# Kernel optimization log

Measured on AMD Instinct MI355X. Metric: run time of the kernel, lower is better.

## Reference

```python
import jax, jax.numpy as jnp
import numpy as np

D_MODEL = 1024
N_HEADS = 16
D_K = D_MODEL // N_HEADS
THETA = 10000.0
SEQ = 2048
BATCH = 2


def setup_inputs() -> dict:
    key = jax.random.key(0)
    ks = jax.random.split(key, 5)
    std = (2.0 / (D_MODEL + D_MODEL)) ** 0.5
    return {
        "x": jax.random.normal(ks[0], (BATCH, SEQ, D_MODEL), dtype=jnp.float32),
        "token_positions": jnp.arange(SEQ, dtype=jnp.int64 if jax.config.jax_enable_x64 else jnp.int32),
        "wq": jax.random.normal(ks[1], (D_MODEL, D_MODEL), dtype=jnp.float32) * std,
        "wk": jax.random.normal(ks[2], (D_MODEL, D_MODEL), dtype=jnp.float32) * std,
        "wv": jax.random.normal(ks[3], (D_MODEL, D_MODEL), dtype=jnp.float32) * std,
        "wo": jax.random.normal(ks[4], (D_MODEL, D_MODEL), dtype=jnp.float32) * std,
    }


def _apply_rope(t, token_positions):
    # t: [b, h, s, d_k]; interleaved even/odd rotation (RoPE)
    k = jnp.arange(D_K // 2, dtype=t.dtype)
    inv_freq = THETA ** (-2.0 * k / D_K)                     # [d_k/2]
    angles = token_positions.astype(t.dtype)[:, None] * inv_freq  # [s, d_k/2]
    cos, sin = jnp.cos(angles), jnp.sin(angles)
    even, odd = t[..., 0::2], t[..., 1::2]
    re = even * cos - odd * sin
    ro = odd * cos + even * sin
    # re-interleave: stack last then reshape back to [..., d_k]
    return jnp.stack([re, ro], axis=-1).reshape(t.shape)


def reference(x, token_positions, wq, wk, wv, wo):
    b, s, _ = x.shape
    def proj(w):
        y = jnp.einsum("bsd,ed->bse", x, w)               # Linear: x @ W^T
        return y.reshape(b, s, N_HEADS, D_K).transpose(0, 2, 1, 3)  # [b,h,s,dk]
    q, k, v = proj(wq), proj(wk), proj(wv)
    q = _apply_rope(q, token_positions)
    k = _apply_rope(k, token_positions)
    scores = jnp.einsum("bhqd,bhkd->bhqk", q, k) / jnp.sqrt(jnp.asarray(D_K, x.dtype))
    attn = jax.nn.softmax(scores, axis=-1)
    out = jnp.einsum("bhqk,bhkd->bhqd", attn, v)          # [b,h,s,dk]
    out = out.transpose(0, 2, 1, 3).reshape(b, s, D_MODEL)
    return jnp.einsum("bsd,ed->bse", out, wo)
```

## Files before the change

kernel.cpp:

```cpp
#include <hip/hip_runtime.h>
#include <stdint.h>

typedef __bf16 bf16x8 __attribute__((ext_vector_type(8)));
typedef __bf16 bf16x2 __attribute__((ext_vector_type(2)));
typedef float f32x4 __attribute__((ext_vector_type(4)));
typedef float f32x16 __attribute__((ext_vector_type(16)));
typedef unsigned short ushort_t;
typedef unsigned int uint;

#define SEQ    2048
#define DMODEL 1024
#define NHEAD  16
#define DKH    64
#define NBATCH 2
#define MROWS  (NBATCH*SEQ)
#define LOG2E  1.44269504088896340736f

__device__ __forceinline__ uint pk2(float a, float b) {
  bf16x2 t; t[0] = (__bf16)a; t[1] = (__bf16)b;
  return __builtin_bit_cast(uint, t);
}
__device__ __forceinline__ ushort_t b1(float a) {
  return __builtin_bit_cast(ushort_t, (__bf16)a);
}
__device__ __forceinline__ float fexp2(float x) {
#if __has_builtin(__builtin_amdgcn_exp2f)
  return __builtin_amdgcn_exp2f(x);
#else
  return exp2f(x);
#endif
}

__device__ __forceinline__ void gload16(const void* g, void* l) {
  __builtin_amdgcn_global_load_lds(
      (const __attribute__((address_space(1))) void*)g,
      (__attribute__((address_space(3))) void*)l, 16, 0, 0);
}

__device__ __forceinline__ f32x4 mfma16(bf16x8 a, bf16x8 b, f32x4 c) {
  return __builtin_amdgcn_mfma_f32_16x16x32_bf16(a, b, c, 0, 0, 0);
}
__device__ __forceinline__ f32x16 mfma32(bf16x8 a, bf16x8 b, f32x16 c) {
  return __builtin_amdgcn_mfma_f32_32x32x16_bf16(a, b, c, 0, 0, 0);
}

__global__ __launch_bounds__(256) void cvt_all(
    const float* __restrict__ x, const float* __restrict__ wq,
    const float* __restrict__ wk, const float* __restrict__ wv,
    const float* __restrict__ wo, uint2* __restrict__ out)
{
  int b = blockIdx.x;
  const float4* src; uint2* dst; int i;
  if (b < 4096) {
    i = b * 256 + threadIdx.x; src = (const float4*)x; dst = out;
  } else {
    int s = (b - 4096) >> 10;
    i = ((b - 4096) & 1023) * 256 + threadIdx.x;
    src = (const float4*)(s == 0 ? wq : s == 1 ? wk : s == 2 ? wv : wo);
    dst = out + (size_t)1048576 + (size_t)s * 262144;
  }
  float4 v = src[i];
  uint2 r; r.x = pk2(v.x, v.y); r.y = pk2(v.z, v.w);
  dst[i] = r;
}

__global__ __launch_bounds__(256) void rope_tab_kernel(const int* __restrict__ tokpos, float2* __restrict__ tab) {
  int t = blockIdx.x * 256 + threadIdx.x;
  int s = t >> 5, k = t & 31;
  double inv = pow(10000.0, -(double)(2 * k) / 64.0);
  double ang = (double)tokpos[s] * inv;
  tab[t] = make_float2((float)cos(ang), (float)sin(ang));
}

__global__ __launch_bounds__(256) void gemm_nt(
    const ushort_t* __restrict__ A, const ushort_t* __restrict__ W,
    const float2* __restrict__ tab,
    ushort_t* __restrict__ Qo, ushort_t* __restrict__ Ko, ushort_t* __restrict__ Vo,
    float* __restrict__ outf, int fused)
{
  __shared__ ushort_t lA[2][128 * 64];
  __shared__ ushort_t lB[2][128 * 64];
  const int tid = threadIdx.x;
  const int w = tid >> 6, l = tid & 63, lo = l & 15, hi = l >> 4;
  const int wr = (w >> 1) * 64, wc = (w & 1) * 64;
  const char* Ab = (const char*)A + (size_t)blockIdx.y * 128 * 2048;
  const char* Bb = (const char*)W + (size_t)blockIdx.x * 128 * 2048;
  f32x4 acc[4][4] = {};

  const int o0 = w * 1024 + l * 16;
  const int r0 = o0 >> 7;
  const int us = ((o0 >> 4) & 7) ^ (r0 & 7);
  const char* ap = Ab + (size_t)r0 * 2048 + us * 16;
  const char* bp = Bb + (size_t)r0 * 2048 + us * 16;

  auto stage = [&](char* dA, char* dB, const char* aq, const char* bq) {
    #pragma unroll
    for (int i = 0; i < 4; ++i) {
      gload16(aq + i * 65536, dA + w * 1024 + i * 4096);
      gload16(bq + i * 65536, dB + w * 1024 + i * 4096);
    }
  };
  auto comp = [&](const ushort_t* lAb, const ushort_t* lBb) {
    #pragma unroll
    for (int c = 0; c < 2; ++c) {
      bf16x8 af[4], wf[4];
      #pragma unroll
      for (int m = 0; m < 4; ++m) {
        int row = wr + m * 16 + lo;
        af[m] = *(const bf16x8*)((const char*)lAb + row * 128 + ((c * 64 + hi * 16) ^ ((row & 7) << 4)));
      }
      #pragma unroll
      for (int n = 0; n < 4; ++n) {
        int row = wc + n * 16 + lo;
        wf[n] = *(const bf16x8*)((const char*)lBb + row * 128 + ((c * 64 + hi * 16) ^ ((row & 7) << 4)));
      }
      #pragma unroll
      for (int m = 0; m < 4; ++m)
        #pragma unroll
        for (int n = 0; n < 4; ++n)
          acc[m][n] = mfma16(af[m], wf[n], acc[m][n]);
    }
  };

  stage((char*)lA[0], (char*)lB[0], ap, bp); ap += 128; bp += 128;
  __syncthreads();
  for (int it = 0; it < 16; it += 2) {
    stage((char*)lA[1], (char*)lB[1], ap, bp); ap += 128; bp += 128;
    comp(lA[0], lB[0]);
    __syncthreads();
    if (it + 2 < 16) { stage((char*)lA[0], (char*)lB[0], ap, bp); ap += 128; bp += 128; }
    comp(lA[1], lB[1]);
    __syncthreads();
  }

  const int mode = fused ? (blockIdx.x >> 3) : 3;
  const int colblk = fused ? (blockIdx.x & 7) : blockIdx.x;
  const int rowbase = blockIdx.y * 128 + wr + hi * 4;
  const int colbase = colblk * 128 + wc + lo;

  if (mode == 3) {
    #pragma unroll
    for (int m = 0; m < 4; ++m)
      #pragma unroll
      for (int n = 0; n < 4; ++n) {
        int e = colbase + n * 16;
        #pragma unroll
        for (int r = 0; r < 4; ++r) {
          int row = rowbase + m * 16 + r;
          outf[(size_t)row * 1024 + e] = acc[m][n][r];
        }
      }
    return;
  }
  if (mode == 2) {
    #pragma unroll
    for (int m = 0; m < 4; ++m) {
      int row0 = rowbase + m * 16;
      int b = row0 >> 11, s = row0 & 2047;
      #pragma unroll
      for (int n = 0; n < 4; ++n) {
        int e = colbase + n * 16;
        int h = e >> 6, dk = e & 63;
        uint2 pk;
        pk.x = pk2(acc[m][n][0], acc[m][n][1]);
        pk.y = pk2(acc[m][n][2], acc[m][n][3]);
        *(uint2*)(Vo + ((size_t)((b * NHEAD + h) * DKH + dk) * SEQ + s)) = pk;
      }
    }
    return;
  }
  ushort_t* outb = (mode == 0) ? Qo : Ko;
  const float qscale = (mode == 0) ? (0.125f * LOG2E) : 1.0f;
  #pragma unroll
  for (int m = 0; m < 4; ++m) {
    #pragma unroll
    for (int n = 0; n < 4; ++n) {
      int e = colbase + n * 16;
      int h = e >> 6, dk = e & 63, kf = dk >> 1;
      float sgn = (e & 1) ? 1.0f : -1.0f;
      #pragma unroll
      for (int r = 0; r < 4; ++r) {
        int row = rowbase + m * 16 + r;
        int s = row & 2047, b = row >> 11;
        float2 cs = tab[s * 32 + kf];
        float v = acc[m][n][r];
        float p = __shfl_xor(v, 1, 64);
        float res = (v * cs.x + sgn * p * cs.y) * qscale;
        outb[((size_t)((b * NHEAD + h) * SEQ + s)) * DKH + dk] = b1(res);
      }
    }
  }
}

__global__ __launch_bounds__(128) void attn_fwd(
    const ushort_t* __restrict__ Qg, const ushort_t* __restrict__ Kg,
    const ushort_t* __restrict__ VTg, ushort_t* __restrict__ attn)
{
  __shared__ char lds[65536];
  const int tid = threadIdx.x;
  const int w = tid >> 6, l = tid & 63;
  const int q31 = l & 31, hf = l >> 5, s7 = l & 7;
  const int bh = blockIdx.y;
  const int q0 = blockIdx.x * 128 + w * 64;
  const char* Kb = (const char*)Kg + (size_t)bh * 2048 * 128;
  const char* Vb = (const char*)VTg + (size_t)bh * 64 * 4096;

  bf16x8 qreg[2][4];
  #pragma unroll
  for (int qb = 0; qb < 2; ++qb) {
    const ushort_t* qp = Qg + ((size_t)bh * 2048 + q0 + qb * 32 + q31) * 64 + hf * 8;
    #pragma unroll
    for (int c = 0; c < 4; ++c) qreg[qb][c] = *(const bf16x8*)(qp + c * 16);
  }

  f32x16 accO[2][2] = {};
  float lsum[2] = {0.f, 0.f};

  const char* ra[4];
  #pragma unroll
  for (int c = 0; c < 4; ++c)
    ra[c] = lds + q31 * 128 + ((c * 32 + hf * 16) ^ (s7 << 4));
  const int lPoff = 49152 + w * 8192;
  char* wbase = lds + lPoff + q31 * 128 + hf * 8;

  const int su = (tid & 7) ^ ((tid >> 3) & 7);
  const char* kp = Kb + (size_t)(tid >> 3) * 128 + su * 16;
  const char* vp = Vb + (size_t)(tid >> 3) * 4096 + su * 16;

  auto stageT = [&](int bufo) {
    #pragma unroll
    for (int i = 0; i < 4; ++i)
      gload16(kp + i * 2048, lds + bufo + i * 2048 + tid * 16);
    #pragma unroll
    for (int i = 0; i < 4; ++i)
      gload16(vp + i * 65536, lds + bufo + 8192 + i * 2048 + tid * 16);
    kp += 8192; vp += 128;
  };

  auto tileC = [&](int bo) {
    #pragma unroll
    for (int kb = 0; kb < 2; ++kb) {
      bf16x8 kf[4];
      #pragma unroll
      for (int c = 0; c < 4; ++c)
        kf[c] = *(const bf16x8*)(ra[c] + bo + kb * 4096);
      f32x16 s0 = {}, s1 = {};
      #pragma unroll
      for (int c = 0; c < 4; ++c) {
        s0 = mfma32(kf[c], qreg[0][c], s0);
        s1 = mfma32(kf[c], qreg[1][c], s1);
      }
      float p0[16], p1[16];
      float t0 = 0.f, t1 = 0.f;
      #pragma unroll
      for (int r = 0; r < 16; ++r) { p0[r] = fexp2(s0[r]); t0 += p0[r]; }
      #pragma unroll
      for (int r = 0; r < 16; ++r) { p1[r] = fexp2(s1[r]); t1 += p1[r]; }
      lsum[0] += t0; lsum[1] += t1;
      #pragma unroll
      for (int g2 = 0; g2 < 4; ++g2) {
        uint2 pk;
        pk.x = pk2(p0[g2 * 4 + 0], p0[g2 * 4 + 1]);
        pk.y = pk2(p0[g2 * 4 + 2], p0[g2 * 4 + 3]);
        *(uint2*)(wbase + ((kb * 64 + g2 * 16) ^ (s7 << 4))) = pk;
      }
      #pragma unroll
      for (int g2 = 0; g2 < 4; ++g2) {
        uint2 pk;
        pk.x = pk2(p1[g2 * 4 + 0], p1[g2 * 4 + 1]);
        pk.y = pk2(p1[g2 * 4 + 2], p1[g2 * 4 + 3]);
        *(uint2*)(wbase + 4096 + ((kb * 64 + g2 * 16) ^ (s7 << 4))) = pk;
      }
      #pragma unroll
      for (int kcl = 0; kcl < 2; ++kcl) {
        int kc = kb * 2 + kcl;
        bf16x8 vf0 = *(const bf16x8*)(ra[kc] + bo + 8192);
        bf16x8 vf1 = *(const bf16x8*)(ra[kc] + bo + 8192 + 4096);
        bf16x8 pb0 = *(const bf16x8*)(ra[kc] + lPoff);
        bf16x8 pb1 = *(const bf16x8*)(ra[kc] + lPoff + 4096);
        accO[0][0] = mfma32(vf0, pb0, accO[0][0]);
        accO[0][1] = mfma32(vf1, pb0, accO[0][1]);
        accO[1][0] = mfma32(vf0, pb1, accO[1][0]);
        accO[1][1] = mfma32(vf1, pb1, accO[1][1]);
      }
    }
  };

  stageT(0);
  stageT(16384);
  #pragma unroll 1
  for (int it = 0; it < 10; ++it) {
    #pragma unroll
    for (int j = 0; j < 3; ++j) {
      asm volatile("s_waitcnt vmcnt(8)" ::: "memory");
      __builtin_amdgcn_s_barrier();
      __builtin_amdgcn_sched_barrier(0);
      stageT(((j + 2) % 3) * 16384);
      tileC(j * 16384);
    }
  }
  asm volatile("s_waitcnt vmcnt(8)" ::: "memory");
  __builtin_amdgcn_s_barrier();
  __builtin_amdgcn_sched_barrier(0);
  tileC(0);
  asm volatile("s_waitcnt vmcnt(0)" ::: "memory");
  __builtin_amdgcn_s_barrier();
  __builtin_amdgcn_sched_barrier(0);
  tileC(16384);

  int b = bh >> 4, head = bh & 15;
  #pragma unroll
  for (int qb = 0; qb < 2; ++qb) {
    float lt = lsum[qb] + __shfl_xor(lsum[qb], 32, 64);
    float inv = 1.0f / lt;
    ushort_t* op = attn + (size_t)(b * 2048 + q0 + qb * 32 + q31) * 1024 + head * 64;
    #pragma unroll
    for (int db = 0; db < 2; ++db)
      #pragma unroll
      for (int m = 0; m < 4; ++m) {
        int d0 = db * 32 + m * 8 + hf * 4;
        uint2 pk;
        pk.x = pk2(accO[qb][db][m * 4 + 0] * inv, accO[qb][db][m * 4 + 1] * inv);
        pk.y = pk2(accO[qb][db][m * 4 + 2] * inv, accO[qb][db][m * 4 + 3] * inv);
        *(uint2*)(op + d0) = pk;
      }
  }
}

extern "C" void kernel_launch(void* const* d_in, const int* in_sizes, int n_in,
                              void* d_out, int out_size, void* d_ws, size_t ws_size,
                              hipStream_t stream) {
  const float* x  = (const float*)d_in[0];
  const int* tok  = (const int*)d_in[1];
  const float* wq = (const float*)d_in[2];
  const float* wk = (const float*)d_in[3];
  const float* wv = (const float*)d_in[4];
  const float* wo = (const float*)d_in[5];
  float* out = (float*)d_out;
  char* ws = (char*)d_ws;

  size_t off = 0;
  float2* tab = (float2*)(ws + off); off += (size_t)SEQ * 32 * sizeof(float2);
  ushort_t* xb  = (ushort_t*)(ws + off); off += (size_t)MROWS * DMODEL * 2;
  ushort_t* wqkv = (ushort_t*)(ws + off); off += (size_t)3 * DMODEL * DMODEL * 2;
  ushort_t* wob = (ushort_t*)(ws + off); off += (size_t)DMODEL * DMODEL * 2;
  ushort_t* Qg  = (ushort_t*)(ws + off); off += (size_t)MROWS * DMODEL * 2;
  ushort_t* Kg  = (ushort_t*)(ws + off); off += (size_t)MROWS * DMODEL * 2;
  ushort_t* VTg = (ushort_t*)(ws + off); off += (size_t)MROWS * DMODEL * 2;
  ushort_t* attnb = xb;
  if (ws_size < off) return;

  cvt_all<<<8192, 256, 0, stream>>>(x, wq, wk, wv, wo, (uint2*)xb);
  rope_tab_kernel<<<256, 256, 0, stream>>>(tok, tab);

  gemm_nt<<<dim3(24, 32), 256, 0, stream>>>(xb, wqkv, tab, Qg, Kg, VTg, nullptr, 1);

  attn_fwd<<<dim3(SEQ / 128, NBATCH * NHEAD), 128, 0, stream>>>(Qg, Kg, VTg, attnb);

  gemm_nt<<<dim3(8, 32), 256, 0, stream>>>(attnb, wob, nullptr, nullptr, nullptr, nullptr, out, 0);
}
```

Baseline: 133.0 us.

## Split attention key range across two wave pairs and reduce partials in LDS

The attention kernel now launches 256 threads per block. Two waves cover each 64-query slice, and each processes half of every 64-key tile, which changes the staging layout for K/V tiles. Their partial O accumulators and row sums are combined through LDS at the end. This doubles the waves working on each query block, for more latency hiding and MFMA issue parallelism per CU, at the cost of 80KB of LDS, an extra reduction with two syncthreads, and possibly lower block occupancy.

```diff
diff --git a/kernel.cpp b/kernel.cpp
--- a/kernel.cpp
+++ b/kernel.cpp
@@ -192,16 +192,17 @@
   }
 }
 
-__global__ __launch_bounds__(128) void attn_fwd(
+__global__ __launch_bounds__(256) void attn_fwd(
     const ushort_t* __restrict__ Qg, const ushort_t* __restrict__ Kg,
     const ushort_t* __restrict__ VTg, ushort_t* __restrict__ attn)
 {
-  __shared__ char lds[65536];
+  __shared__ char lds[81920];
   const int tid = threadIdx.x;
   const int w = tid >> 6, l = tid & 63;
+  const int qh = w >> 1, kp = w & 1;
   const int q31 = l & 31, hf = l >> 5, s7 = l & 7;
   const int bh = blockIdx.y;
-  const int q0 = blockIdx.x * 128 + w * 64;
+  const int q0 = blockIdx.x * 128 + qh * 64;
   const char* Kb = (const char*)Kg + (size_t)bh * 2048 * 128;
   const char* Vb = (const char*)VTg + (size_t)bh * 64 * 4096;
 
@@ -220,69 +221,66 @@
   #pragma unroll
   for (int c = 0; c < 4; ++c)
     ra[c] = lds + q31 * 128 + ((c * 32 + hf * 16) ^ (s7 << 4));
-  const int lPoff = 49152 + w * 8192;
-  char* wbase = lds + lPoff + q31 * 128 + hf * 8;
-
-  const int su = (tid & 7) ^ ((tid >> 3) & 7);
-  const char* kp = Kb + (size_t)(tid >> 3) * 128 + su * 16;
-  const char* vp = Vb + (size_t)(tid >> 3) * 4096 + su * 16;
-
-  auto stageT = [&](int bufo) {
-    #pragma unroll
-    for (int i = 0; i < 4; ++i)
-      gload16(kp + i * 2048, lds + bufo + i * 2048 + tid * 16);
-    #pragma unroll
-    for (int i = 0; i < 4; ++i)
-      gload16(vp + i * 65536, lds + bufo + 8192 + i * 2048 + tid * 16);
-    kp += 8192; vp += 128;
+  const int lP = 49152 + w * 8192;
+  char* wb = lds + lP + q31 * 128 + hf * 8;
+  const int bq = kp * 8192;
+
+  const int srow = tid >> 3, sw = (tid & 7) * 16;
+  const int wl = sw ^ ((srow & 7) << 4);
+  const char* ksp = Kb + (size_t)srow * 128 + wl;
+  const char* vsp = Vb + (size_t)(srow + ((wl >> 6) & 1) * 32) * 4096 + (wl & 63);
+
+  auto stageT = [&](int slot) {
+    gload16(ksp,        lds + slot + tid * 16);
+    gload16(ksp + 4096, lds + slot + 8192 + tid * 16);
+    gload16(vsp,        lds + slot + 4096 + tid * 16);
+    gload16(vsp + 64,   lds + slot + 12288 + tid * 16);
+    ksp += 8192; vsp += 128;
   };
 
-  auto tileC = [&](int bo) {
-    #pragma unroll
-    for (int kb = 0; kb < 2; ++kb) {
-      bf16x8 kf[4];
-      #pragma unroll
-      for (int c = 0; c < 4; ++c)
-        kf[c] = *(const bf16x8*)(ra[c] + bo + kb * 4096);
-      f32x16 s0 = {}, s1 = {};
-      #pragma unroll
-      for (int c = 0; c < 4; ++c) {
-        s0 = mfma32(kf[c], qreg[0][c], s0);
-        s1 = mfma32(kf[c], qreg[1][c], s1);
-      }
-      float p0[16], p1[16];
-      float t0 = 0.f, t1 = 0.f;
-      #pragma unroll
-      for (int r = 0; r < 16; ++r) { p0[r] = fexp2(s0[r]); t0 += p0[r]; }
-      #pragma unroll
-      for (int r = 0; r < 16; ++r) { p1[r] = fexp2(s1[r]); t1 += p1[r]; }
-      lsum[0] += t0; lsum[1] += t1;
-      #pragma unroll
-      for (int g2 = 0; g2 < 4; ++g2) {
-        uint2 pk;
-        pk.x = pk2(p0[g2 * 4 + 0], p0[g2 * 4 + 1]);
-        pk.y = pk2(p0[g2 * 4 + 2], p0[g2 * 4 + 3]);
-        *(uint2*)(wbase + ((kb * 64 + g2 * 16) ^ (s7 << 4))) = pk;
-      }
-      #pragma unroll
-      for (int g2 = 0; g2 < 4; ++g2) {
-        uint2 pk;
-        pk.x = pk2(p1[g2 * 4 + 0], p1[g2 * 4 + 1]);
-        pk.y = pk2(p1[g2 * 4 + 2], p1[g2 * 4 + 3]);
-        *(uint2*)(wbase + 4096 + ((kb * 64 + g2 * 16) ^ (s7 << 4))) = pk;
-      }
-      #pragma unroll
-      for (int kcl = 0; kcl < 2; ++kcl) {
-        int kc = kb * 2 + kcl;
-        bf16x8 vf0 = *(const bf16x8*)(ra[kc] + bo + 8192);
-        bf16x8 vf1 = *(const bf16x8*)(ra[kc] + bo + 8192 + 4096);
-        bf16x8 pb0 = *(const bf16x8*)(ra[kc] + lPoff);
-        bf16x8 pb1 = *(const bf16x8*)(ra[kc] + lPoff + 4096);
-        accO[0][0] = mfma32(vf0, pb0, accO[0][0]);
-        accO[0][1] = mfma32(vf1, pb0, accO[0][1]);
-        accO[1][0] = mfma32(vf0, pb1, accO[1][0]);
-        accO[1][1] = mfma32(vf1, pb1, accO[1][1]);
-      }
+  auto tileC = [&](int slot) {
+    const int bo = slot + bq;
+    bf16x8 kf[4];
+    #pragma unroll
+    for (int c = 0; c < 4; ++c)
+      kf[c] = *(const bf16x8*)(ra[c] + bo);
+    f32x16 s0 = {}, s1 = {};
+    #pragma unroll
+    for (int c = 0; c < 4; ++c) {
+      s0 = mfma32(kf[c], qreg[0][c], s0);
+      s1 = mfma32(kf[c], qreg[1][c], s1);
+    }
+    float p0[16], p1[16];
+    float t0 = 0.f, t1 = 0.f;
+    #pragma unroll
+    for (int r = 0; r < 16; ++r) { p0[r] = fexp2(s0[r]); t0 += p0[r]; }
+    #pragma unroll
+    for (int r = 0; r < 16; ++r) { p1[r] = fexp2(s1[r]); t1 += p1[r]; }
+    lsum[0] += t0; lsum[1] += t1;
+    #pragma unroll
+    for (int g2 = 0; g2 < 4; ++g2) {
+      uint2 pk;
+      pk.x = pk2(p0[g2 * 4 + 0], p0[g2 * 4 + 1]);
+      pk.y = pk2(p0[g2 * 4 + 2], p0[g2 * 4 + 3]);
+      *(uint2*)(wb + ((g2 * 16) ^ (s7 << 4))) = pk;
+    }
+    #pragma unroll
+    for (int g2 = 0; g2 < 4; ++g2) {
+      uint2 pk;
+      pk.x = pk2(p1[g2 * 4 + 0], p1[g2 * 4 + 1]);
+      pk.y = pk2(p1[g2 * 4 + 2], p1[g2 * 4 + 3]);
+      *(uint2*)(wb + 4096 + ((g2 * 16) ^ (s7 << 4))) = pk;
+    }
+    #pragma unroll
+    for (int kcl = 0; kcl < 2; ++kcl) {
+      bf16x8 pb0 = *(const bf16x8*)(ra[kcl] + lP);
+      bf16x8 pb1 = *(const bf16x8*)(ra[kcl] + lP + 4096);
+      bf16x8 vf0 = *(const bf16x8*)(ra[kcl]     + bo + 4096);
+      bf16x8 vf1 = *(const bf16x8*)(ra[kcl + 2] + bo + 4096);
+      accO[0][0] = mfma32(vf0, pb0, accO[0][0]);
+      accO[0][1] = mfma32(vf1, pb0, accO[0][1]);
+      accO[1][0] = mfma32(vf0, pb1, accO[1][0]);
+      accO[1][1] = mfma32(vf1, pb1, accO[1][1]);
     }
   };
 
@@ -292,14 +290,14 @@
   for (int it = 0; it < 10; ++it) {
     #pragma unroll
     for (int j = 0; j < 3; ++j) {
-      asm volatile("s_waitcnt vmcnt(8)" ::: "memory");
+      asm volatile("s_waitcnt vmcnt(4)" ::: "memory");
       __builtin_amdgcn_s_barrier();
       __builtin_amdgcn_sched_barrier(0);
       stageT(((j + 2) % 3) * 16384);
       tileC(j * 16384);
     }
   }
-  asm volatile("s_waitcnt vmcnt(8)" ::: "memory");
+  asm volatile("s_waitcnt vmcnt(4)" ::: "memory");
   __builtin_amdgcn_s_barrier();
   __builtin_amdgcn_sched_barrier(0);
   tileC(0);
@@ -308,22 +306,58 @@
   __builtin_amdgcn_sched_barrier(0);
   tileC(16384);
 
-  int b = bh >> 4, head = bh & 15;
-  #pragma unroll
-  for (int qb = 0; qb < 2; ++qb) {
-    float lt = lsum[qb] + __shfl_xor(lsum[qb], 32, 64);
-    float inv = 1.0f / lt;
-    ushort_t* op = attn + (size_t)(b * 2048 + q0 + qb * 32 + q31) * 1024 + head * 64;
-    #pragma unroll
-    for (int db = 0; db < 2; ++db)
-      #pragma unroll
-      for (int m = 0; m < 4; ++m) {
-        int d0 = db * 32 + m * 8 + hf * 4;
-        uint2 pk;
-        pk.x = pk2(accO[qb][db][m * 4 + 0] * inv, accO[qb][db][m * 4 + 1] * inv);
-        pk.y = pk2(accO[qb][db][m * 4 + 2] * inv, accO[qb][db][m * 4 + 3] * inv);
-        *(uint2*)(op + d0) = pk;
-      }
+  __syncthreads();
+  if (kp) {
+    char* dst = lds + qh * 16384;
+    #pragma unroll
+    for (int qb = 0; qb < 2; ++qb)
+      #pragma unroll
+      for (int db = 0; db < 2; ++db)
+        #pragma unroll
+        for (int c2 = 0; c2 < 4; ++c2) {
+          int j = qb * 8 + db * 4 + c2;
+          f32x4 v = { accO[qb][db][c2 * 4 + 0], accO[qb][db][c2 * 4 + 1],
+                      accO[qb][db][c2 * 4 + 2], accO[qb][db][c2 * 4 + 3] };
+          *(f32x4*)(dst + j * 1024 + l * 16) = v;
+        }
+    *(float2*)(lds + 32768 + qh * 512 + l * 8) = make_float2(lsum[0], lsum[1]);
+  }
+  __syncthreads();
+  if (!kp) {
+    const char* srcp = lds + qh * 16384;
+    #pragma unroll
+    for (int qb = 0; qb < 2; ++qb)
+      #pragma unroll
+      for (int db = 0; db < 2; ++db)
+        #pragma unroll
+        for (int c2 = 0; c2 < 4; ++c2) {
+          int j = qb * 8 + db * 4 + c2;
+          f32x4 v = *(const f32x4*)(srcp + j * 1024 + l * 16);
+          accO[qb][db][c2 * 4 + 0] += v[0];
+          accO[qb][db][c2 * 4 + 1] += v[1];
+          accO[qb][db][c2 * 4 + 2] += v[2];
+          accO[qb][db][c2 * 4 + 3] += v[3];
+        }
+    float2 lo = *(const float2*)(lds + 32768 + qh * 512 + l * 8);
+    lsum[0] += lo.x; lsum[1] += lo.y;
+
+    int b = bh >> 4, head = bh & 15;
+    #pragma unroll
+    for (int qb = 0; qb < 2; ++qb) {
+      float lt = lsum[qb] + __shfl_xor(lsum[qb], 32, 64);
+      float inv = 1.0f / lt;
+      ushort_t* op = attn + (size_t)(b * 2048 + q0 + qb * 32 + q31) * 1024 + head * 64;
+      #pragma unroll
+      for (int db = 0; db < 2; ++db)
+        #pragma unroll
+        for (int m = 0; m < 4; ++m) {
+          int d0 = db * 32 + m * 8 + hf * 4;
+          uint2 pk;
+          pk.x = pk2(accO[qb][db][m * 4 + 0] * inv, accO[qb][db][m * 4 + 1] * inv);
+          pk.y = pk2(accO[qb][db][m * 4 + 2] * inv, accO[qb][db][m * 4 + 3] * inv);
+          *(uint2*)(op + d0) = pk;
+        }
+    }
   }
 }
 
@@ -355,7 +389,7 @@
 
   gemm_nt<<<dim3(24, 32), 256, 0, stream>>>(xb, wqkv, tab, Qg, Kg, VTg, nullptr, 1);
 
-  attn_fwd<<<dim3(SEQ / 128, NBATCH * NHEAD), 128, 0, stream>>>(Qg, Kg, VTg, attnb);
+  attn_fwd<<<dim3(SEQ / 128, NBATCH * NHEAD), 256, 0, stream>>>(Qg, Kg, VTg, attnb);
 
   gemm_nt<<<dim3(8, 32), 256, 0, stream>>>(attnb, wob, nullptr, nullptr, nullptr, nullptr, out, 0);
 }
```

New measurement: 129.5 us. -2.6%, faster.
